# Kernel tuning notes

Measured on AMD Instinct MI355X. Metric: run time of the kernel, lower is better.

The kernel has to match this reference:

```python
import jax, jax.numpy as jnp
import numpy as np

NUM_HEADS = 16
HEAD_DIM = 128  # 2048 // 16


def setup_inputs() -> dict:
    key = jax.random.key(0)
    ks = jax.random.split(key, 5)
    B, S, D = 2, 2048, 2048
    scale = 0.02
    return {
        "inputs": jax.random.normal(ks[0], (B, S, D), dtype=jnp.float32),
        "attention_mask": jnp.ones((B, S), dtype=jnp.float32),
        "Wq": jax.random.normal(ks[1], (D, D), dtype=jnp.float32) * scale,
        "Wk": jax.random.normal(ks[2], (D, D), dtype=jnp.float32) * scale,
        "Wv": jax.random.normal(ks[3], (D, D), dtype=jnp.float32) * scale,
        "Wo": jax.random.normal(ks[4], (D, D), dtype=jnp.float32) * scale,
    }


def reference(inputs, attention_mask, Wq, Wk, Wv, Wo):
    B, S, D = inputs.shape
    H, Dh = NUM_HEADS, HEAD_DIM

    def proj(W):
        # nn.Linear: x @ W.T -> [B,S,H,Dh] -> [B,H,S,Dh]
        return (inputs @ W.T).reshape(B, S, H, Dh).transpose(0, 2, 1, 3)

    q, k, v = proj(Wq), proj(Wk), proj(Wv)

    scores = jnp.einsum("bhqd,bhkd->bhqk", q, k) * (1.0 / jnp.sqrt(jnp.float32(Dh)))

    # ALiBi bias: slopes[h] * (pos_q - pos_k), subtracted from scores
    slopes = 2.0 ** (-8.0 * jnp.arange(1, H + 1, dtype=jnp.float32) / H)
    pos = jnp.arange(S, dtype=jnp.float32)
    pos_diff = pos[:, None] - pos[None, :]              # [S,S]
    scores = scores - slopes[None, :, None, None] * pos_diff[None, None, :, :]

    # causal mask: add -inf above the diagonal
    causal = jnp.where(jnp.triu(jnp.ones((S, S), dtype=bool), k=1), -jnp.inf, 0.0)
    scores = scores + causal[None, None, :, :]

    # original multiplies scores by the mask (broadcast over key axis)
    scores = scores * attention_mask[:, None, None, :]

    weights = jax.nn.softmax(scores, axis=-1)
    attn = jnp.einsum("bhqk,bhkd->bhqd", weights, v)
    attn = attn.transpose(0, 2, 1, 3).reshape(B, S, D)
    return attn @ Wo.T
```

## Files before the change

### kernel.cpp

```cpp
#include <hip/hip_runtime.h>
#include <hip/hip_bf16.h>
#include <stdint.h>

using bf16 = __bf16;
using bf16x8 = __attribute__((ext_vector_type(8))) __bf16;
using bf16x4 = __attribute__((ext_vector_type(4))) __bf16;
using f32x4  = __attribute__((ext_vector_type(4))) float;
using u16x8  = __attribute__((ext_vector_type(8))) unsigned short;

#define MFMA16(a,b,c) __builtin_amdgcn_mfma_f32_16x16x32_bf16((a),(b),(c),0,0,0)

__device__ __forceinline__ void gll16(const void* g, void* l) {
  __builtin_amdgcn_global_load_lds(
      (const __attribute__((address_space(1))) uint32_t*)g,
      (__attribute__((address_space(3))) uint32_t*)l, 16, 0, 0);
}

__global__ __launch_bounds__(256) void f32_to_bf16_k(
    const float* __restrict__ in, bf16* __restrict__ out, int n4) {
  int i = blockIdx.x * blockDim.x + threadIdx.x;
  if (i >= n4) return;
  const float4 v = ((const float4*)in)[i];
  bf16x4 o;
  o[0] = (bf16)v.x; o[1] = (bf16)v.y; o[2] = (bf16)v.z; o[3] = (bf16)v.w;
  ((bf16x4*)out)[i] = o;
}

template <typename OutT>
__global__ __launch_bounds__(256, 2) void gemm_bt(
    const bf16* __restrict__ A,
    const bf16* __restrict__ B0, const bf16* __restrict__ B1, const bf16* __restrict__ B2,
    OutT* __restrict__ C0, OutT* __restrict__ C1, OutT* __restrict__ C2,
    int M, int N, int K) {
  const int gx = gridDim.x, gy = gridDim.y;
  const int nwg = gx * gy * gridDim.z;
  int lid = blockIdx.x + gx * (blockIdx.y + gy * blockIdx.z);
  lid = (lid & 7) * (nwg >> 3) + (lid >> 3);
  const int bz = lid / (gx * gy);
  const int rem = lid - bz * (gx * gy);
  const int by = rem / gx, bx = rem - by * gx;

  const bf16* Bm = (bz == 0) ? B0 : (bz == 1 ? B1 : B2);
  OutT* C = (bz == 0) ? C0 : (bz == 1 ? C1 : C2);

  __shared__ bf16 As[128 * 32];
  __shared__ bf16 Bs[128 * 32];

  const int t = threadIdx.x;
  const int w = t >> 6;
  const int l = t & 63;
  const int m0 = by * 128;
  const int n0 = bx * 128;
  const int wr = (w >> 1) * 64;
  const int wc = (w & 1) * 64;

  f32x4 acc[4][4] = {};

  const int srow = w * 32 + (l >> 2);
  const int scol = (l & 3) * 8;
  const bf16* Ag = A + (int64_t)(m0 + srow) * K + scol;
  const bf16* Bg = Bm + (int64_t)(n0 + srow) * K + scol;

  const int ar = (l & 15) * 32 + (l >> 4) * 8;

  for (int k0 = 0; k0 < K; k0 += 32) {
    gll16(Ag + k0,          As + (w * 2 + 0) * 512);
    gll16(Ag + k0 + 16 * K, As + (w * 2 + 1) * 512);
    gll16(Bg + k0,          Bs + (w * 2 + 0) * 512);
    gll16(Bg + k0 + 16 * K, Bs + (w * 2 + 1) * 512);
    __syncthreads();

    bf16x8 af[4], bfr[4];
#pragma unroll
    for (int mi = 0; mi < 4; ++mi) af[mi] = *(const bf16x8*)&As[(wr + mi * 16) * 32 + ar];
#pragma unroll
    for (int ni = 0; ni < 4; ++ni) bfr[ni] = *(const bf16x8*)&Bs[(wc + ni * 16) * 32 + ar];
#pragma unroll
    for (int mi = 0; mi < 4; ++mi)
#pragma unroll
      for (int ni = 0; ni < 4; ++ni)
        acc[mi][ni] = MFMA16(af[mi], bfr[ni], acc[mi][ni]);
    __syncthreads();
  }

#pragma unroll
  for (int mi = 0; mi < 4; ++mi) {
    const int row = m0 + wr + mi * 16 + (l >> 4) * 4;
#pragma unroll
    for (int ni = 0; ni < 4; ++ni) {
      const int col = n0 + wc + ni * 16 + (l & 15);
#pragma unroll
      for (int j = 0; j < 4; ++j)
        C[(int64_t)(row + j) * N + col] = (OutT)acc[mi][ni][j];
    }
  }
}

__global__ __launch_bounds__(256, 2) void attn_fwd(
    const bf16* __restrict__ Q, const bf16* __restrict__ Kb,
    const bf16* __restrict__ V, const float* __restrict__ mask,
    bf16* __restrict__ O) {
  constexpr int S = 2048, D = 2048, Dh = 128;
  __shared__ bf16 Ks[2][64 * 128];
  __shared__ bf16 Vt[2][128 * 64];
  __shared__ bf16 Pl[4][16 * 68];

  const int t = threadIdx.x, w = t >> 6, l = t & 63;
  const int lq = l & 15, lk = l >> 4;

  const int nwg = gridDim.x * gridDim.y;
  int lid = blockIdx.x + gridDim.x * blockIdx.y;
  lid = (lid & 7) * (nwg >> 3) + (lid >> 3);
  const int bx = lid & 31, by = lid >> 5;

  const int qt = 31 - bx;
  const int q0 = qt * 64;
  const int b = by >> 4, h = by & 15;
  const int swz = (lq & 7) << 4;

  const int kvp = t & 31;
  const int d80 = (t >> 5) * 8;
  const int d81 = d80 + 64;

  bf16x8 qf[4];
  {
    const bf16* Qrow = Q + (int64_t)(b * S + q0 + w * 16 + lq) * D + h * Dh;
#pragma unroll
    for (int kk = 0; kk < 4; ++kk) qf[kk] = *(const bf16x8*)&Qrow[kk * 32 + lk * 8];
  }

  float mr = -1e30f, lr = 0.f;
  f32x4 oacc[8] = {};

  const float scale = 0.08838834764831845f;
  const float slope = exp2f(-0.5f * (float)(h + 1));
  const int ntiles = qt + 1;
  const int qrow = q0 + w * 16 + lq;

  bf16x8 vA0, vA1, vB0, vB1;

#define LOAD_V(kt)                                                          \
  {                                                                         \
    const bf16* vb = V + (int64_t)(b * S + (kt) * 64 + 2 * kvp) * D + h * Dh; \
    vA0 = *(const bf16x8*)(vb + d80);                                       \
    vA1 = *(const bf16x8*)(vb + D + d80);                                   \
    vB0 = *(const bf16x8*)(vb + d81);                                       \
    vB1 = *(const bf16x8*)(vb + D + d81);                                   \
  }

#define STAGE_K(kt, buf)                                                    \
  {                                                                         \
    _Pragma("unroll")                                                       \
    for (int i = 0; i < 4; ++i) {                                           \
      const int chunk = 4 * w + i;                                          \
      const int r = chunk * 4 + (l >> 4);                                   \
      const int cbl = ((l & 15) * 16) ^ ((r & 7) << 4);                     \
      gll16(Kb + (int64_t)(b * S + (kt) * 64 + r) * D + h * Dh + (cbl >> 1),\
            &Ks[buf][chunk * 512]);                                         \
    }                                                                       \
  }

#define WRITE_V(buf)                                                        \
  {                                                                         \
    const u16x8 u00 = __builtin_bit_cast(u16x8, vA0);                       \
    const u16x8 u01 = __builtin_bit_cast(u16x8, vA1);                       \
    const u16x8 u10 = __builtin_bit_cast(u16x8, vB0);                       \
    const u16x8 u11 = __builtin_bit_cast(u16x8, vB1);                       \
    char* vtb = (char*)&Vt[buf][0];                                         \
    _Pragma("unroll")                                                       \
    for (int jj = 0; jj < 8; ++jj) {                                        \
      const int co = (4 * kvp) ^ (jj << 4);                                 \
      *(uint32_t*)(vtb + (d80 + jj) * 128 + co) =                           \
          (uint32_t)u00[jj] | ((uint32_t)u01[jj] << 16);                    \
      *(uint32_t*)(vtb + (d81 + jj) * 128 + co) =                           \
          (uint32_t)u10[jj] | ((uint32_t)u11[jj] << 16);                    \
    }                                                                       \
  }

  LOAD_V(0);
  STAGE_K(0, 0);
  WRITE_V(0);
  __syncthreads();

  for (int kt = 0; kt < ntiles; ++kt) {
    const int cb = kt & 1, nb = cb ^ 1;
    const int kv0 = kt * 64;
    const bool pft = (kt + 1 < ntiles);
    if (pft) {
      STAGE_K(kt + 1, nb);
      LOAD_V(kt + 1);
    }

    f32x4 sc[4];
#pragma unroll
    for (int ni = 0; ni < 4; ++ni) {
      const char* krow = (const char*)&Ks[cb][(ni * 16 + lq) * 128];
      f32x4 a = {};
#pragma unroll
      for (int kk = 0; kk < 4; ++kk) {
        bf16x8 kf = *(const bf16x8*)(krow + ((kk * 64 + lk * 16) ^ swz));
        a = MFMA16(kf, qf[kk], a);
      }
      sc[ni] = a;
    }

#pragma unroll
    for (int ni = 0; ni < 4; ++ni) {
      const float4 mv = *(const float4*)&mask[b * S + kv0 + ni * 16 + lk * 4];
      const float* mvp = (const float*)&mv;
#pragma unroll
      for (int j = 0; j < 4; ++j) {
        const int kcol = kv0 + ni * 16 + lk * 4 + j;
        float s = sc[ni][j] * scale - slope * (float)(qrow - kcol);
        s = (kcol > qrow) ? -1e30f : s;
        sc[ni][j] = s * mvp[j];
      }
    }

    float mj = sc[0][0];
#pragma unroll
    for (int ni = 0; ni < 4; ++ni)
#pragma unroll
      for (int j = 0; j < 4; ++j) mj = fmaxf(mj, sc[ni][j]);
    mj = fmaxf(mj, __shfl_xor(mj, 16));
    mj = fmaxf(mj, __shfl_xor(mj, 32));
    const float mnew = fmaxf(mr, mj);
    const float r = __expf(mr - mnew);
    mr = mnew;
    float ps = 0.f;
#pragma unroll
    for (int ni = 0; ni < 4; ++ni)
#pragma unroll
      for (int j = 0; j < 4; ++j) {
        const float p = __expf(sc[ni][j] - mnew);
        sc[ni][j] = p;
        ps += p;
      }
    ps += __shfl_xor(ps, 16);
    ps += __shfl_xor(ps, 32);
    lr = lr * r + ps;
#pragma unroll
    for (int df = 0; df < 8; ++df)
#pragma unroll
      for (int j = 0; j < 4; ++j) oacc[df][j] *= r;

#pragma unroll
    for (int ni = 0; ni < 4; ++ni) {
      bf16x4 pb;
#pragma unroll
      for (int j = 0; j < 4; ++j) pb[j] = (bf16)sc[ni][j];
      *(bf16x4*)&Pl[w][lq * 68 + ni * 16 + lk * 4] = pb;
    }

    bf16x8 pf0 = *(const bf16x8*)&Pl[w][lq * 68 + lk * 8];
    bf16x8 pf1 = *(const bf16x8*)&Pl[w][lq * 68 + 32 + lk * 8];

#pragma unroll
    for (int df = 0; df < 8; ++df) {
      const char* vrow = (const char*)&Vt[cb][(df * 16 + lq) * 64];
      bf16x8 vf0 = *(const bf16x8*)(vrow + ((lk * 16) ^ swz));
      oacc[df] = MFMA16(vf0, pf0, oacc[df]);
      bf16x8 vf1 = *(const bf16x8*)(vrow + ((64 + lk * 16) ^ swz));
      oacc[df] = MFMA16(vf1, pf1, oacc[df]);
    }

    if (pft) WRITE_V(nb);
    __syncthreads();
  }

  const float inv = 1.0f / lr;
  bf16* orow = O + (int64_t)(b * S + qrow) * D + h * Dh;
#pragma unroll
  for (int df = 0; df < 8; ++df) {
    bf16x4 ob;
#pragma unroll
    for (int j = 0; j < 4; ++j) ob[j] = (bf16)(oacc[df][j] * inv);
    *(bf16x4*)&orow[df * 16 + lk * 4] = ob;
  }
#undef LOAD_V
#undef STAGE_K
#undef WRITE_V
}

extern "C" void kernel_launch(void* const* d_in, const int* in_sizes, int n_in,
                              void* d_out, int out_size, void* d_ws, size_t ws_size,
                              hipStream_t stream) {
  const float* X    = (const float*)d_in[0];
  const float* mask = (const float*)d_in[1];
  const float* Wq   = (const float*)d_in[2];
  const float* Wk   = (const float*)d_in[3];
  const float* Wv   = (const float*)d_in[4];
  const float* Wo   = (const float*)d_in[5];
  float* out = (float*)d_out;

  bf16* ws = (bf16*)d_ws;
  bf16* Xb  = ws;
  bf16* Wqb = ws + 8388608;
  bf16* Wkb = ws + 12582912;
  bf16* Wvb = ws + 16777216;
  bf16* Wob = ws + 20971520;
  bf16* Qb  = ws + 25165824;
  bf16* Kb  = ws + 33554432;
  bf16* Vb  = ws + 41943040;
  bf16* Ab  = ws + 50331648;

  f32_to_bf16_k<<<8192, 256, 0, stream>>>(X,  Xb,  2097152);
  f32_to_bf16_k<<<4096, 256, 0, stream>>>(Wq, Wqb, 1048576);
  f32_to_bf16_k<<<4096, 256, 0, stream>>>(Wk, Wkb, 1048576);
  f32_to_bf16_k<<<4096, 256, 0, stream>>>(Wv, Wvb, 1048576);
  f32_to_bf16_k<<<4096, 256, 0, stream>>>(Wo, Wob, 1048576);

  gemm_bt<bf16><<<dim3(16, 32, 3), 256, 0, stream>>>(
      Xb, Wqb, Wkb, Wvb, Qb, Kb, Vb, 4096, 2048, 2048);

  attn_fwd<<<dim3(32, 32), 256, 0, stream>>>(Qb, Kb, Vb, mask, Ab);

  gemm_bt<float><<<dim3(16, 32, 1), 256, 0, stream>>>(
      Ab, Wob, Wob, Wob, out, out, out, 4096, 2048, 2048);
}
```

Baseline: 435.3 us.

## Double-buffer larger GEMM tiles, fuse casts, use exp2 with lazy softmax rescale

Replaces the five fp32-to-bf16 launches with one combined conversion kernel. Rewrites the projection GEMM to 256x128 tiles with BK=64, 512 threads, a double-buffered LDS ring with an XOR swizzle, split prefetch and MFMA priority hints. In attention it folds log2(e) into scale and slope so it can use exp2, and skips the rescale of the running max and accumulator unless the max grows beyond a threshold. Larger tiles use more LDS and registers and lower occupancy, and the lazy rescale relies on fp32 headroom.

```diff
diff --git a/kernel.cpp b/kernel.cpp
--- a/kernel.cpp
+++ b/kernel.cpp
@@ -16,18 +16,27 @@
       (__attribute__((address_space(3))) uint32_t*)l, 16, 0, 0);
 }
 
-__global__ __launch_bounds__(256) void f32_to_bf16_k(
-    const float* __restrict__ in, bf16* __restrict__ out, int n4) {
-  int i = blockIdx.x * blockDim.x + threadIdx.x;
-  if (i >= n4) return;
-  const float4 v = ((const float4*)in)[i];
+__global__ __launch_bounds__(256) void cvt_all_k(
+    const float* __restrict__ X, const float* __restrict__ Wq,
+    const float* __restrict__ Wk, const float* __restrict__ Wv,
+    const float* __restrict__ Wo, bf16* __restrict__ Xb,
+    bf16* __restrict__ Wqb, bf16* __restrict__ Wkb,
+    bf16* __restrict__ Wvb, bf16* __restrict__ Wob) {
+  const int i = blockIdx.x * blockDim.x + threadIdx.x;
+  const float* src; bf16* dst; int off;
+  if (i < 2097152)      { src = X;  dst = Xb;  off = i; }
+  else if (i < 3145728) { src = Wq; dst = Wqb; off = i - 2097152; }
+  else if (i < 4194304) { src = Wk; dst = Wkb; off = i - 3145728; }
+  else if (i < 5242880) { src = Wv; dst = Wvb; off = i - 4194304; }
+  else                  { src = Wo; dst = Wob; off = i - 5242880; }
+  const float4 v = ((const float4*)src)[off];
   bf16x4 o;
   o[0] = (bf16)v.x; o[1] = (bf16)v.y; o[2] = (bf16)v.z; o[3] = (bf16)v.w;
-  ((bf16x4*)out)[i] = o;
+  ((bf16x4*)dst)[off] = o;
 }
 
 template <typename OutT>
-__global__ __launch_bounds__(256, 2) void gemm_bt(
+__global__ __launch_bounds__(512, 1) void gemm_bt(
     const bf16* __restrict__ A,
     const bf16* __restrict__ B0, const bf16* __restrict__ B1, const bf16* __restrict__ B2,
     OutT* __restrict__ C0, OutT* __restrict__ C1, OutT* __restrict__ C2,
@@ -43,57 +52,112 @@
   const bf16* Bm = (bz == 0) ? B0 : (bz == 1 ? B1 : B2);
   OutT* C = (bz == 0) ? C0 : (bz == 1 ? C1 : C2);
 
-  __shared__ bf16 As[128 * 32];
-  __shared__ bf16 Bs[128 * 32];
+  __shared__ bf16 As[2][256 * 64];
+  __shared__ bf16 Bs[2][128 * 64];
 
   const int t = threadIdx.x;
-  const int w = t >> 6;
-  const int l = t & 63;
-  const int m0 = by * 128;
-  const int n0 = bx * 128;
-  const int wr = (w >> 1) * 64;
-  const int wc = (w & 1) * 64;
-
-  f32x4 acc[4][4] = {};
-
-  const int srow = w * 32 + (l >> 2);
-  const int scol = (l & 3) * 8;
-  const bf16* Ag = A + (int64_t)(m0 + srow) * K + scol;
-  const bf16* Bg = Bm + (int64_t)(n0 + srow) * K + scol;
-
-  const int ar = (l & 15) * 32 + (l >> 4) * 8;
-
-  for (int k0 = 0; k0 < K; k0 += 32) {
-    gll16(Ag + k0,          As + (w * 2 + 0) * 512);
-    gll16(Ag + k0 + 16 * K, As + (w * 2 + 1) * 512);
-    gll16(Bg + k0,          Bs + (w * 2 + 0) * 512);
-    gll16(Bg + k0 + 16 * K, Bs + (w * 2 + 1) * 512);
-    __syncthreads();
-
-    bf16x8 af[4], bfr[4];
-#pragma unroll
-    for (int mi = 0; mi < 4; ++mi) af[mi] = *(const bf16x8*)&As[(wr + mi * 16) * 32 + ar];
-#pragma unroll
-    for (int ni = 0; ni < 4; ++ni) bfr[ni] = *(const bf16x8*)&Bs[(wc + ni * 16) * 32 + ar];
-#pragma unroll
-    for (int mi = 0; mi < 4; ++mi)
-#pragma unroll
-      for (int ni = 0; ni < 4; ++ni)
-        acc[mi][ni] = MFMA16(af[mi], bfr[ni], acc[mi][ni]);
-    __syncthreads();
-  }
-
-#pragma unroll
-  for (int mi = 0; mi < 4; ++mi) {
-    const int row = m0 + wr + mi * 16 + (l >> 4) * 4;
-#pragma unroll
-    for (int ni = 0; ni < 4; ++ni) {
-      const int col = n0 + wc + ni * 16 + (l & 15);
+  const int w = t >> 6, l = t & 63;
+  const int wm = w >> 2, wn = w & 3;
+  const int m0 = by * 256, n0 = bx * 128;
+
+  const int lr8 = l >> 3;
+  const int sc8 = ((l & 7) ^ lr8) * 8;
+  const bf16* Agl = A  + (int64_t)(m0 + w * 32 + lr8) * K + sc8;
+  const bf16* Bgl = Bm + (int64_t)(n0 + w * 16 + lr8) * K + sc8;
+
+#define STAGE_A(kc, buf, i) \
+  gll16(Agl + (int64_t)((i) * 8) * K + (kc), (char*)&As[buf][0] + (w * 4 + (i)) * 1024)
+#define STAGE_B(kc, buf, i) \
+  gll16(Bgl + (int64_t)((i) * 8) * K + (kc), (char*)&Bs[buf][0] + (w * 2 + (i)) * 1024)
+
+  const int swzR = (l & 7) << 4;
+  const int g0   = (l >> 4) * 16;
+  const int rowA = wm * 128 + (l & 15);
+  const int rowB = wn * 32 + (l & 15);
+
+  f32x4 acc[8][2] = {};
+
+  STAGE_A(0, 0, 0); STAGE_A(0, 0, 1); STAGE_B(0, 0, 0);
+  STAGE_A(0, 0, 2); STAGE_A(0, 0, 3); STAGE_B(0, 0, 1);
+
+  const int KT = K >> 6;
+  for (int kt = 0; kt < KT; ++kt) {
+    const int cb = kt & 1, nb = cb ^ 1;
+    const int kc = (kt + 1) << 6;
+    const bool pf = (kt + 1 < KT);
+
+    if (pf) {
+      STAGE_A(kc, nb, 0); STAGE_A(kc, nb, 1); STAGE_B(kc, nb, 0);
+      asm volatile("s_waitcnt vmcnt(3)" ::: "memory");
+    } else {
+      asm volatile("s_waitcnt vmcnt(0)" ::: "memory");
+    }
+    __builtin_amdgcn_s_barrier();
+    asm volatile("" ::: "memory");
+
+    const char* AsB = (const char*)&As[cb][0] + rowA * 128;
+    const char* BsB = (const char*)&Bs[cb][0] + rowB * 128;
+
+    bf16x8 b_[2][2];
+#pragma unroll
+    for (int ni = 0; ni < 2; ++ni)
+#pragma unroll
+      for (int kk = 0; kk < 2; ++kk)
+        b_[ni][kk] = *(const bf16x8*)(BsB + ni * 2048 + ((g0 + kk * 64) ^ swzR));
+
+    {
+      bf16x8 a_[4][2];
+#pragma unroll
+      for (int mi = 0; mi < 4; ++mi)
+#pragma unroll
+        for (int kk = 0; kk < 2; ++kk)
+          a_[mi][kk] = *(const bf16x8*)(AsB + mi * 2048 + ((g0 + kk * 64) ^ swzR));
+      __builtin_amdgcn_s_setprio(1);
+#pragma unroll
+      for (int kk = 0; kk < 2; ++kk)
+#pragma unroll
+        for (int mi = 0; mi < 4; ++mi)
+#pragma unroll
+          for (int ni = 0; ni < 2; ++ni)
+            acc[mi][ni] = MFMA16(a_[mi][kk], b_[ni][kk], acc[mi][ni]);
+      __builtin_amdgcn_s_setprio(0);
+    }
+
+    if (pf) { STAGE_A(kc, nb, 2); STAGE_A(kc, nb, 3); STAGE_B(kc, nb, 1); }
+    {
+      bf16x8 a_[4][2];
+#pragma unroll
+      for (int mi = 0; mi < 4; ++mi)
+#pragma unroll
+        for (int kk = 0; kk < 2; ++kk)
+          a_[mi][kk] = *(const bf16x8*)(AsB + (4 + mi) * 2048 + ((g0 + kk * 64) ^ swzR));
+      __builtin_amdgcn_s_setprio(1);
+#pragma unroll
+      for (int kk = 0; kk < 2; ++kk)
+#pragma unroll
+        for (int mi = 0; mi < 4; ++mi)
+#pragma unroll
+          for (int ni = 0; ni < 2; ++ni)
+            acc[4 + mi][ni] = MFMA16(a_[mi][kk], b_[ni][kk], acc[4 + mi][ni]);
+      __builtin_amdgcn_s_setprio(0);
+    }
+    asm volatile("" ::: "memory");
+    __builtin_amdgcn_s_barrier();
+  }
+
+#pragma unroll
+  for (int mi = 0; mi < 8; ++mi) {
+    const int row = m0 + wm * 128 + mi * 16 + (l >> 4) * 4;
+#pragma unroll
+    for (int ni = 0; ni < 2; ++ni) {
+      const int col = n0 + wn * 32 + ni * 16 + (l & 15);
 #pragma unroll
       for (int j = 0; j < 4; ++j)
         C[(int64_t)(row + j) * N + col] = (OutT)acc[mi][ni][j];
     }
   }
+#undef STAGE_A
+#undef STAGE_B
 }
 
 __global__ __launch_bounds__(256, 2) void attn_fwd(
@@ -132,8 +196,9 @@
   float mr = -1e30f, lr = 0.f;
   f32x4 oacc[8] = {};
 
-  const float scale = 0.08838834764831845f;
-  const float slope = exp2f(-0.5f * (float)(h + 1));
+  constexpr float LOG2E = 1.4426950408889634f;
+  const float scale2 = 0.08838834764831845f * LOG2E;
+  const float slope2 = exp2f(-0.5f * (float)(h + 1)) * LOG2E;
   const int ntiles = qt + 1;
   const int qrow = q0 + w * 16 + lq;
 
@@ -211,7 +276,7 @@
 #pragma unroll
       for (int j = 0; j < 4; ++j) {
         const int kcol = kv0 + ni * 16 + lk * 4 + j;
-        float s = sc[ni][j] * scale - slope * (float)(qrow - kcol);
+        float s = sc[ni][j] * scale2 - slope2 * (float)(qrow - kcol);
         s = (kcol > qrow) ? -1e30f : s;
         sc[ni][j] = s * mvp[j];
       }
@@ -224,25 +289,28 @@
       for (int j = 0; j < 4; ++j) mj = fmaxf(mj, sc[ni][j]);
     mj = fmaxf(mj, __shfl_xor(mj, 16));
     mj = fmaxf(mj, __shfl_xor(mj, 32));
-    const float mnew = fmaxf(mr, mj);
-    const float r = __expf(mr - mnew);
-    mr = mnew;
+    if (!__all(mj - mr <= 11.5f)) {
+      const float mnew = fmaxf(mr, mj);
+      const float r2 = exp2f(mr - mnew);
+      lr *= r2;
+#pragma unroll
+      for (int df = 0; df < 8; ++df)
+#pragma unroll
+        for (int j = 0; j < 4; ++j) oacc[df][j] *= r2;
+      mr = mnew;
+    }
     float ps = 0.f;
 #pragma unroll
     for (int ni = 0; ni < 4; ++ni)
 #pragma unroll
       for (int j = 0; j < 4; ++j) {
-        const float p = __expf(sc[ni][j] - mnew);
+        const float p = exp2f(sc[ni][j] - mr);
         sc[ni][j] = p;
         ps += p;
       }
     ps += __shfl_xor(ps, 16);
     ps += __shfl_xor(ps, 32);
-    lr = lr * r + ps;
-#pragma unroll
-    for (int df = 0; df < 8; ++df)
-#pragma unroll
-      for (int j = 0; j < 4; ++j) oacc[df][j] *= r;
+    lr += ps;
 
 #pragma unroll
     for (int ni = 0; ni < 4; ++ni) {
@@ -304,17 +372,14 @@
   bf16* Vb  = ws + 41943040;
   bf16* Ab  = ws + 50331648;
 
-  f32_to_bf16_k<<<8192, 256, 0, stream>>>(X,  Xb,  2097152);
-  f32_to_bf16_k<<<4096, 256, 0, stream>>>(Wq, Wqb, 1048576);
-  f32_to_bf16_k<<<4096, 256, 0, stream>>>(Wk, Wkb, 1048576);
-  f32_to_bf16_k<<<4096, 256, 0, stream>>>(Wv, Wvb, 1048576);
-  f32_to_bf16_k<<<4096, 256, 0, stream>>>(Wo, Wob, 1048576);
-
-  gemm_bt<bf16><<<dim3(16, 32, 3), 256, 0, stream>>>(
+  cvt_all_k<<<24576, 256, 0, stream>>>(X, Wq, Wk, Wv, Wo,
+                                       Xb, Wqb, Wkb, Wvb, Wob);
+
+  gemm_bt<bf16><<<dim3(16, 16, 3), 512, 0, stream>>>(
       Xb, Wqb, Wkb, Wvb, Qb, Kb, Vb, 4096, 2048, 2048);
 
   attn_fwd<<<dim3(32, 32), 256, 0, stream>>>(Qb, Kb, Vb, mask, Ab);
 
-  gemm_bt<float><<<dim3(16, 32, 1), 256, 0, stream>>>(
+  gemm_bt<float><<<dim3(16, 16, 1), 512, 0, stream>>>(
       Ab, Wob, Wob, Wob, out, out, out, 4096, 2048, 2048);
 }
```

Result: slower. 456.2 us (+4.8%).
